# Optimization experiments

Hardware: AMD Instinct MI355X
Metric: run time of the kernel (lower is better)

The kernel has to match this reference:

```python
import jax, jax.numpy as jnp
import numpy as np

N, E = 20000, 160000
H, C1, C_OUT, D_IN = 4, 256, 512, 128
HID = H * C1  # 1024


def gat_conv(x, src, dst, W, a_src, a_dst, b, heads, ch, concat):
    n = x.shape[0]
    xw = (x @ W).reshape(n, heads, ch)                     # [N,H,C]
    es = jnp.sum(xw * a_src, axis=-1)                      # [N,H]
    ed = jnp.sum(xw * a_dst, axis=-1)                      # [N,H]
    e = jax.nn.leaky_relu(es[src] + ed[dst], 0.2)          # [Etot,H]
    m = jax.ops.segment_max(e, dst, num_segments=n)
    m = jnp.where(jnp.isfinite(m), m, 0.0)
    p = jnp.exp(e - m[dst])
    denom = jax.ops.segment_sum(p, dst, num_segments=n)
    alpha = p / (denom[dst] + 1e-16)                       # segment softmax
    out = jax.ops.segment_sum(alpha[:, :, None] * xw[src], dst, num_segments=n)
    out = out.reshape(n, heads * ch) if concat else out.mean(axis=1)
    return out + b


def layer_norm(x, g, b, eps=1e-5):
    mu = jnp.mean(x, axis=-1, keepdims=True)
    var = jnp.var(x, axis=-1, keepdims=True)
    return (x - mu) * jax.lax.rsqrt(var + eps) * g + b


def setup_inputs() -> dict:
    key = jax.random.key(0)
    ks = jax.random.split(key, 16)
    s1, s2, s3 = (2.0 / D_IN) ** 0.5, (2.0 / HID) ** 0.5, (2.0 / HID) ** 0.5
    return {
        "x": jax.random.normal(ks[0], (N, D_IN), jnp.float32),
        "edge_index": jax.random.randint(ks[1], (2, E), 0, N, jnp.int64),
        "W1": jax.random.normal(ks[2], (D_IN, H * C1), jnp.float32) * s1,
        "a_src1": jax.random.normal(ks[3], (H, C1), jnp.float32) * 0.1,
        "a_dst1": jax.random.normal(ks[4], (H, C1), jnp.float32) * 0.1,
        "b1": jnp.zeros((HID,), jnp.float32),
        "ln1_g": jnp.ones((HID,), jnp.float32),
        "ln1_b": jnp.zeros((HID,), jnp.float32),
        "W2": jax.random.normal(ks[5], (HID, H * C1), jnp.float32) * s2,
        "a_src2": jax.random.normal(ks[6], (H, C1), jnp.float32) * 0.1,
        "a_dst2": jax.random.normal(ks[7], (H, C1), jnp.float32) * 0.1,
        "b2": jnp.zeros((HID,), jnp.float32),
        "ln2_g": jnp.ones((HID,), jnp.float32),
        "ln2_b": jnp.zeros((HID,), jnp.float32),
        "W3": jax.random.normal(ks[8], (HID, C_OUT), jnp.float32) * s3,
        "a_src3": jax.random.normal(ks[9], (1, C_OUT), jnp.float32) * 0.1,
        "a_dst3": jax.random.normal(ks[10], (1, C_OUT), jnp.float32) * 0.1,
        "b3": jnp.zeros((C_OUT,), jnp.float32),
    }


def reference(x, edge_index, W1, a_src1, a_dst1, b1, ln1_g, ln1_b,
              W2, a_src2, a_dst2, b2, ln2_g, ln2_b,
              W3, a_src3, a_dst3, b3):
    # add self loops (PyG GATConv default add_self_loops=True)
    loops = jnp.arange(N, dtype=edge_index.dtype)
    src = jnp.concatenate([edge_index[0], loops])
    dst = jnp.concatenate([edge_index[1], loops])

    h = gat_conv(x, src, dst, W1, a_src1, a_dst1, b1, H, C1, True)
    h = jax.nn.elu(layer_norm(h, ln1_g, ln1_b))  # dropout: eval mode (identity)
    h = gat_conv(h, src, dst, W2, a_src2, a_dst2, b2, H, C1, True)
    h = jax.nn.elu(layer_norm(h, ln2_g, ln2_b))
    out = gat_conv(h, src, dst, W3, a_src3, a_dst3, b3, 1, C_OUT, True)
    return out
```

## Files before the change

kernel.cpp:

```cpp
#include <hip/hip_runtime.h>
#include <hip/hip_bf16.h>

typedef __hip_bfloat16 bf16;
typedef __attribute__((ext_vector_type(8))) short short8;
typedef __attribute__((ext_vector_type(4))) float float4v;

#define NN 20000
#define EE 160000
#define ET (NN + EE)

__device__ __forceinline__ float bf2f(bf16 v){ return __bfloat162float(v); }
__device__ __forceinline__ float raw2f(unsigned short u){ return __uint_as_float(((unsigned)u) << 16); }

struct Ptrs { const void* p[18]; int n[18]; };

__global__ void k_detect(Ptrs P, int* __restrict__ flags){
  int b = blockIdx.x;
  int t = threadIdx.x;
  if (b == 1){
    const int* e = (const int*)P.p[1];
    int odd = e[2*t + 1];
    unsigned long long m2 = __ballot(odd != 0);
    if (t == 0){ flags[1] = (m2 == 0ULL) ? 1 : 0; }
    return;
  }
  const unsigned* w = (const unsigned*)P.p[b];
  int nwords = P.n[b] / 2;
  unsigned v = w[t % nwords];
  int e8 = (v >> 7) & 0xFF;
  int looks = (e8 >= 100 && e8 <= 140) ? 1 : 0;
  unsigned long long mz = __ballot(v == 0u);
  unsigned long long ml = __ballot(looks);
  if (t == 0){
    int nz = __popcll(mz);
    int nonz = 64 - nz;
    int nl = __popcll(ml);
    flags[8+b] = (nonz > 0 && 2*nl >= nonz) ? 0 : 1;
  }
}

struct P13 { const void* src[13]; int off[13]; int n[13]; int fi[13]; };
struct PrepArgs {
  const void* xraw; bf16* Xc;
  const void* w1raw; bf16* Wt1;
  const void* w2raw; bf16* Wt2;
  const void* w3raw; bf16* Wt3;
  const int* eiraw; int* eic;
  P13 p13; float* prm;
  int* counts;
  const int* flags;
};

__device__ __forceinline__ void do_transpose(float (*tile)[33], const void* raw,
    bf16* wt, int K, int M, int f, int bx, int by, int t){
  int kb = by*32, mb = bx*32;
  int tx = t & 31, ty = t >> 5;
  for (int r = 0; r < 4; r++){
    int k = kb + ty + r*8;
    int m = mb + tx;
    float v = f ? ((const float*)raw)[(size_t)k*M+m] : bf2f(((const bf16*)raw)[(size_t)k*M+m]);
    tile[ty + r*8][tx] = v;
  }
  __syncthreads();
  for (int r = 0; r < 4; r++){
    int m = mb + ty + r*8;
    int k = kb + tx;
    wt[(size_t)m*K + k] = __float2bfloat16(tile[tx][ty + r*8]);
  }
}

__global__ __launch_bounds__(256) void k_prep(PrepArgs A){
  __shared__ float tile[32][33];
  int b = blockIdx.x, t = threadIdx.x;
  const int* flags = A.flags;
  if (b < 10000){
    int i = b*256 + t;
    if (flags[8+0]) A.Xc[i] = __float2bfloat16(((const float*)A.xraw)[i]);
    else            A.Xc[i] = ((const bf16*)A.xraw)[i];
  } else if (b < 10128){
    int r = b - 10000;
    do_transpose(tile, A.w1raw, A.Wt1, 128, 1024, flags[8+2], r & 31, r >> 5, t);
  } else if (b < 11152){
    int r = b - 10128;
    do_transpose(tile, A.w2raw, A.Wt2, 1024, 1024, flags[8+8], r & 31, r >> 5, t);
  } else if (b < 11664){
    int r = b - 11152;
    do_transpose(tile, A.w3raw, A.Wt3, 1024, 512, flags[8+14], r & 15, r >> 4, t);
  } else if (b < 12914){
    int i = (b - 11664)*256 + t;
    if (i < 2*EE) A.eic[i] = flags[1] ? A.eiraw[2*i] : A.eiraw[i];
  } else if (b < 12927){
    int pb = b - 12914;
    const void* s = A.p13.src[pb];
    int n = A.p13.n[pb];
    float* d = A.prm + A.p13.off[pb];
    int f = flags[8 + A.p13.fi[pb]];
    for (int i = t; i < n; i += 256)
      d[i] = f ? ((const float*)s)[i] : bf2f(((const bf16*)s)[i]);
  } else {
    int i = (b - 12927)*256 + t;
    if (i < NN) A.counts[i] = 1;
  }
}

__global__ void k_hist(const int* __restrict__ ei, int* __restrict__ counts){
  int e = blockIdx.x*256 + threadIdx.x;
  if (e < EE){
    int d = ei[EE + e];
    if (d >= 0 && d < NN) atomicAdd(&counts[d], 1);
  }
}

__global__ __launch_bounds__(1024) void k_scan(const int* __restrict__ counts, int* __restrict__ rp){
  __shared__ int wsum[16];
  __shared__ int sc;
  int t = threadIdx.x, lane = t & 63, wv = t >> 6;
  if (t == 0) sc = 0;
  __syncthreads();
  for (int base = 0; base < NN; base += 1024){
    int i = base + t;
    int v = (i < NN) ? counts[i] : 0;
    int x = v;
    #pragma unroll
    for (int o = 1; o < 64; o <<= 1){
      int y = __shfl_up(x, o, 64);
      if (lane >= o) x += y;
    }
    if (lane == 63) wsum[wv] = x;
    __syncthreads();
    if (wv == 0 && lane < 16){
      int w = wsum[lane];
      #pragma unroll
      for (int o = 1; o < 16; o <<= 1){
        int y = __shfl_up(w, o, 16);
        if ((lane & 15) >= o) w += y;
      }
      wsum[lane] = w;
    }
    __syncthreads();
    int carry = sc;
    int wpre = (wv > 0) ? wsum[wv-1] : 0;
    if (i < NN) rp[i] = carry + wpre + x - v;
    __syncthreads();
    if (t == 1023) sc = carry + wsum[15];
    __syncthreads();
  }
  if (t == 0) rp[NN] = sc;
}

__global__ void k_selfloop(const int* __restrict__ rp, int* __restrict__ cursor, int* __restrict__ col){
  int i = blockIdx.x*256 + threadIdx.x;
  if (i < NN){ int p = rp[i]; col[p] = i; cursor[i] = p + 1; }
}

__global__ void k_scatter(const int* __restrict__ ei, int* __restrict__ cursor, int* __restrict__ col){
  int e = blockIdx.x*256 + threadIdx.x;
  if (e < EE){
    int s = ei[e], d = ei[EE + e];
    if (d >= 0 && d < NN){
      int pos = atomicAdd(&cursor[d], 1);
      col[pos] = s;
    }
  }
}

__global__ void k_zero2(float* __restrict__ a, float* __restrict__ b, int n){
  int i = blockIdx.x*256 + threadIdx.x;
  if (i < n){ a[i] = 0.f; b[i] = 0.f; }
}

__global__ __launch_bounds__(256) void k_gemm_mfma(
    const bf16* __restrict__ X, const bf16* __restrict__ Wt, bf16* __restrict__ Y,
    const float* __restrict__ as_, const float* __restrict__ ad_,
    float* __restrict__ es, float* __restrict__ ed,
    int K, int M, int C, int H)
{
  __shared__ bf16 Xs[128*32];
  __shared__ bf16 Bs[128*32];
  int ncols = gridDim.x;
  int bid = blockIdx.y * ncols + blockIdx.x;
  int xcd  = bid & 7;
  int rest = bid >> 3;
  int colb = rest % ncols;
  int rowb = xcd + 8 * (rest / ncols);
  int r0 = rowb * 128;
  if (r0 >= NN) return;
  int c0 = colb * 128;

  int tid  = threadIdx.x;
  int wave = tid >> 6, lane = tid & 63;
  int quad = lane >> 4, l15 = lane & 15;
  int wr = (wave >> 1) * 64;
  int wc = (wave & 1) * 64;

  float4v acc[4][4];
  #pragma unroll
  for (int i=0;i<4;i++)
    #pragma unroll
    for (int j=0;j<4;j++)
      acc[i][j] = (float4v){0.f,0.f,0.f,0.f};

  for (int k0 = 0; k0 < K; k0 += 32){
    #pragma unroll
    for (int i = 0; i < 2; i++){
      int ch = i*256 + tid;
      int row = ch >> 2, kp = ch & 3;
      const bf16* gx = X  + (size_t)(r0 + row)*K + k0 + kp*8;
      const bf16* gb = Wt + (size_t)(c0 + row)*K + k0 + kp*8;
      __builtin_amdgcn_global_load_lds(
        (const __attribute__((address_space(1))) unsigned int*)gx,
        (__attribute__((address_space(3))) unsigned int*)(Xs + ch*8), 16, 0, 0);
      __builtin_amdgcn_global_load_lds(
        (const __attribute__((address_space(1))) unsigned int*)gb,
        (__attribute__((address_space(3))) unsigned int*)(Bs + ch*8), 16, 0, 0);
    }
    __syncthreads();

    short8 af[4], bfr[4];
    #pragma unroll
    for (int i = 0; i < 4; i++)
      af[i]  = *(const short8*)(Xs + ((size_t)(wr + i*16 + l15))*32 + quad*8);
    #pragma unroll
    for (int j = 0; j < 4; j++)
      bfr[j] = *(const short8*)(Bs + ((size_t)(wc + j*16 + l15))*32 + quad*8);
    #pragma unroll
    for (int i = 0; i < 4; i++)
      #pragma unroll
      for (int j = 0; j < 4; j++)
        acc[i][j] = __builtin_amdgcn_mfma_f32_16x16x32_bf16(af[i], bfr[j], acc[i][j], 0, 0, 0);
    __syncthreads();
  }

  int h = c0 / C;
  float asv[4], adv[4];
  #pragma unroll
  for (int j = 0; j < 4; j++){
    int colj = c0 + wc + j*16 + l15;
    asv[j] = as_[colj]; adv[j] = ad_[colj];
  }
  #pragma unroll
  for (int i = 0; i < 4; i++){
    int rbase = r0 + wr + i*16 + quad*4;
    #pragma unroll
    for (int rg = 0; rg < 4; rg++){
      int row = rbase + rg;
      bool ok = (row < NN);
      float pe = 0.f, pd = 0.f;
      #pragma unroll
      for (int j = 0; j < 4; j++){
        float v = acc[i][j][rg];
        int colj = c0 + wc + j*16 + l15;
        if (ok) Y[(size_t)row*M + colj] = __float2bfloat16(v);
        pe += v * asv[j];
        pd += v * adv[j];
      }
      #pragma unroll
      for (int o = 1; o < 16; o <<= 1){
        pe += __shfl_xor(pe, o, 64);
        pd += __shfl_xor(pd, o, 64);
      }
      if (ok && l15 == 0){
        atomicAdd(&es[row*H + h], pe);
        atomicAdd(&ed[row*H + h], pd);
      }
    }
  }
}

#define DCAP 1024
__global__ __launch_bounds__(256) void k_aggln(const int* __restrict__ rp, const int* __restrict__ col,
    const bf16* __restrict__ xw, const float* __restrict__ es, const float* __restrict__ ed,
    const float* __restrict__ bias, const float* __restrict__ gam, const float* __restrict__ bet,
    bf16* __restrict__ act){
  int n = blockIdx.x, t = threadIdx.x;
  int h = t >> 6;
  __shared__ float llog[DCAP][4];
  __shared__ int ssrc[DCAP];
  __shared__ float smv[4], srd[4];
  __shared__ float ls1[256], ls2[256];
  int e0 = rp[n], e1 = rp[n+1], deg = e1 - e0;
  float4 ed4 = *(const float4*)&ed[n*4];
  float a0=0.f, a1=0.f, a2=0.f, a3=0.f;
  const unsigned short* xwu = (const unsigned short*)xw;

  if (deg <= DCAP){
    for (int j = t; j < deg; j += 256){
      int s = col[e0 + j];
      ssrc[j] = s;
      float4 e4 = *(const float4*)&es[s*4];
      float v0 = e4.x + ed4.x; llog[j][0] = v0 > 0.f ? v0 : 0.2f*v0;
      float v1 = e4.y + ed4.y; llog[j][1] = v1 > 0.f ? v1 : 0.2f*v1;
      float v2 = e4.z + ed4.z; llog[j][2] = v2 > 0.f ? v2 : 0.2f*v2;
      float v3 = e4.w + ed4.w; llog[j][3] = v3 > 0.f ? v3 : 0.2f*v3;
    }
    __syncthreads();
    if (t < 4){
      float m = -1e30f;
      for (int j = 0; j < deg; j++) m = fmaxf(m, llog[j][t]);
      float den = 0.f;
      for (int j = 0; j < deg; j++) den += __expf(llog[j][t] - m);
      smv[t] = m; srd[t] = 1.f/(den + 1e-16f);
    }
    __syncthreads();
    for (int j = t; j < deg; j += 256){
      #pragma unroll
      for (int hh = 0; hh < 4; hh++)
        llog[j][hh] = __expf(llog[j][hh] - smv[hh]) * srd[hh];
    }
    __syncthreads();
    int j = 0;
    for (; j + 4 <= deg; j += 4){
      int s0=ssrc[j], s1=ssrc[j+1], s2=ssrc[j+2], s3=ssrc[j+3];
      float al0=llog[j][h], al1=llog[j+1][h], al2=llog[j+2][h], al3=llog[j+3][h];
      ushort4 u0 = *(const ushort4*)(xwu + (size_t)s0*1024 + 4*t);
      ushort4 u1 = *(const ushort4*)(xwu + (size_t)s1*1024 + 4*t);
      ushort4 u2 = *(const ushort4*)(xwu + (size_t)s2*1024 + 4*t);
      ushort4 u3 = *(const ushort4*)(xwu + (size_t)s3*1024 + 4*t);
      a0 += al0*raw2f(u0.x); a1 += al0*raw2f(u0.y); a2 += al0*raw2f(u0.z); a3 += al0*raw2f(u0.w);
      a0 += al1*raw2f(u1.x); a1 += al1*raw2f(u1.y); a2 += al1*raw2f(u1.z); a3 += al1*raw2f(u1.w);
      a0 += al2*raw2f(u2.x); a1 += al2*raw2f(u2.y); a2 += al2*raw2f(u2.z); a3 += al2*raw2f(u2.w);
      a0 += al3*raw2f(u3.x); a1 += al3*raw2f(u3.y); a2 += al3*raw2f(u3.z); a3 += al3*raw2f(u3.w);
    }
    for (; j < deg; j++){
      int s = ssrc[j];
      float al = llog[j][h];
      ushort4 u = *(const ushort4*)(xwu + (size_t)s*1024 + 4*t);
      a0 += al*raw2f(u.x); a1 += al*raw2f(u.y); a2 += al*raw2f(u.z); a3 += al*raw2f(u.w);
    }
  } else {
    if (t < 4){
      float m = -1e30f;
      for (int e = e0; e < e1; e++){
        float v = es[col[e]*4 + t] + ed[n*4 + t];
        v = v > 0.f ? v : 0.2f*v;
        m = fmaxf(m, v);
      }
      float den = 0.f;
      for (int e = e0; e < e1; e++){
        float v = es[col[e]*4 + t] + ed[n*4 + t];
        v = v > 0.f ? v : 0.2f*v;
        den += __expf(v - m);
      }
      smv[t] = m; srd[t] = 1.f/(den + 1e-16f);
    }
    __syncthreads();
    float edh = ed[n*4 + h];
    for (int e = e0; e < e1; e++){
      int s = col[e];
      float v = es[s*4 + h] + edh;
      v = v > 0.f ? v : 0.2f*v;
      float al = __expf(v - smv[h]) * srd[h];
      ushort4 u = *(const ushort4*)(xwu + (size_t)s*1024 + 4*t);
      a0 += al*raw2f(u.x); a1 += al*raw2f(u.y); a2 += al*raw2f(u.z); a3 += al*raw2f(u.w);
    }
  }

  a0 += bias[4*t+0]; a1 += bias[4*t+1]; a2 += bias[4*t+2]; a3 += bias[4*t+3];
  float s1 = a0+a1+a2+a3;
  float s2 = a0*a0+a1*a1+a2*a2+a3*a3;
  ls1[t] = s1; ls2[t] = s2;
  __syncthreads();
  for (int o = 128; o > 0; o >>= 1){
    if (t < o){ ls1[t] += ls1[t+o]; ls2[t] += ls2[t+o]; }
    __syncthreads();
  }
  float mu  = ls1[0] * (1.f/1024.f);
  float var = ls2[0] * (1.f/1024.f) - mu*mu;
  float rstd = rsqrtf(fmaxf(var, 0.f) + 1e-5f);
  float v0 = (a0-mu)*rstd*gam[4*t+0] + bet[4*t+0];
  float v1 = (a1-mu)*rstd*gam[4*t+1] + bet[4*t+1];
  float v2 = (a2-mu)*rstd*gam[4*t+2] + bet[4*t+2];
  float v3 = (a3-mu)*rstd*gam[4*t+3] + bet[4*t+3];
  v0 = v0 > 0.f ? v0 : (__expf(v0)-1.f);
  v1 = v1 > 0.f ? v1 : (__expf(v1)-1.f);
  v2 = v2 > 0.f ? v2 : (__expf(v2)-1.f);
  v3 = v3 > 0.f ? v3 : (__expf(v3)-1.f);
  ushort4 o4;
  { bf16 hh2=__float2bfloat16(v0); o4.x=*(unsigned short*)&hh2; }
  { bf16 hh2=__float2bfloat16(v1); o4.y=*(unsigned short*)&hh2; }
  { bf16 hh2=__float2bfloat16(v2); o4.z=*(unsigned short*)&hh2; }
  { bf16 hh2=__float2bfloat16(v3); o4.w=*(unsigned short*)&hh2; }
  *(ushort4*)((unsigned short*)act + (size_t)n*1024 + 4*t) = o4;
}

__global__ __launch_bounds__(256) void k_agg3(const int* __restrict__ rp, const int* __restrict__ col,
    const bf16* __restrict__ xw, const float* __restrict__ es, const float* __restrict__ ed,
    const float* __restrict__ bias, float* __restrict__ out){
  int n = blockIdx.x, t = threadIdx.x;
  __shared__ float llog[DCAP];
  __shared__ int ssrc[DCAP];
  __shared__ float smv, srd;
  int e0 = rp[n], e1 = rp[n+1], deg = e1 - e0;
  float edv = ed[n];
  float a0 = 0.f, a1 = 0.f;
  const unsigned short* xwu = (const unsigned short*)xw;

  if (deg <= DCAP){
    for (int j = t; j < deg; j += 256){
      int s = col[e0 + j];
      ssrc[j] = s;
      float v = es[s] + edv;
      llog[j] = v > 0.f ? v : 0.2f*v;
    }
    __syncthreads();
    if (t == 0){
      float m = -1e30f;
      for (int j = 0; j < deg; j++) m = fmaxf(m, llog[j]);
      float den = 0.f;
      for (int j = 0; j < deg; j++) den += __expf(llog[j] - m);
      smv = m; srd = 1.f/(den + 1e-16f);
    }
    __syncthreads();
    for (int j = t; j < deg; j += 256)
      llog[j] = __expf(llog[j] - smv) * srd;
    __syncthreads();
    int j = 0;
    for (; j + 4 <= deg; j += 4){
      int s0=ssrc[j], s1=ssrc[j+1], s2=ssrc[j+2], s3=ssrc[j+3];
      float al0=llog[j], al1=llog[j+1], al2=llog[j+2], al3=llog[j+3];
      ushort2 u0 = *(const ushort2*)(xwu + (size_t)s0*512 + 2*t);
      ushort2 u1 = *(const ushort2*)(xwu + (size_t)s1*512 + 2*t);
      ushort2 u2 = *(const ushort2*)(xwu + (size_t)s2*512 + 2*t);
      ushort2 u3 = *(const ushort2*)(xwu + (size_t)s3*512 + 2*t);
      a0 += al0*raw2f(u0.x); a1 += al0*raw2f(u0.y);
      a0 += al1*raw2f(u1.x); a1 += al1*raw2f(u1.y);
      a0 += al2*raw2f(u2.x); a1 += al2*raw2f(u2.y);
      a0 += al3*raw2f(u3.x); a1 += al3*raw2f(u3.y);
    }
    for (; j < deg; j++){
      int s = ssrc[j];
      float al = llog[j];
      ushort2 u = *(const ushort2*)(xwu + (size_t)s*512 + 2*t);
      a0 += al*raw2f(u.x); a1 += al*raw2f(u.y);
    }
  } else {
    if (t == 0){
      float m = -1e30f;
      for (int e = e0; e < e1; e++){
        float v = es[col[e]] + edv;
        v = v > 0.f ? v : 0.2f*v;
        m = fmaxf(m, v);
      }
      float den = 0.f;
      for (int e = e0; e < e1; e++){
        float v = es[col[e]] + edv;
        v = v > 0.f ? v : 0.2f*v;
        den += __expf(v - m);
      }
      smv = m; srd = 1.f/(den + 1e-16f);
    }
    __syncthreads();
    for (int e = e0; e < e1; e++){
      int s = col[e];
      float v = es[s] + edv;
      v = v > 0.f ? v : 0.2f*v;
      float al = __expf(v - smv) * srd;
      ushort2 u = *(const ushort2*)(xwu + (size_t)s*512 + 2*t);
      a0 += al*raw2f(u.x); a1 += al*raw2f(u.y);
    }
  }
  out[(size_t)n*512 + 2*t]     = a0 + bias[2*t];
  out[(size_t)n*512 + 2*t + 1] = a1 + bias[2*t+1];
}

__global__ void k_wssmall(float* __restrict__ out, float code){
  if (threadIdx.x == 0) out[0] = code;
}

extern "C" void kernel_launch(void* const* d_in, const int* in_sizes, int n_in,
                              void* d_out, int out_size, void* d_ws, size_t ws_size,
                              hipStream_t stream){
  float* out = (float*)d_out;
  char* ws = (char*)d_ws;

  static const int EXP_SZ[18] = {2560000, 320000, 131072, 1024,1024,1024,1024,1024,
                                 1048576, 1024,1024,1024,1024,1024,
                                 524288, 512,512,512};
  if (n_in != 18){ k_wssmall<<<1,64,0,stream>>>(out, 500.0f*301.0f); return; }
  for (int i = 0; i < 18; i++)
    if (in_sizes[i] != EXP_SZ[i]){ k_wssmall<<<1,64,0,stream>>>(out, 500.0f*302.0f); return; }
  if (out_size != NN*512){ k_wssmall<<<1,64,0,stream>>>(out, 500.0f*303.0f); return; }
  const size_t NEED = 93215360;
  if (ws_size < NEED){ k_wssmall<<<1,64,0,stream>>>(out, 500.0f*304.0f); return; }

  bf16* xw    = (bf16*) (ws);
  bf16* act   = (bf16*) (ws + 40960000);
  bf16* Xc    = (bf16*) (ws + 81920000);
  bf16* Wt1   = (bf16*) (ws + 87040000);
  bf16* Wt2   = (bf16*) (ws + 87302144);
  bf16* Wt3   = (bf16*) (ws + 89399296);
  float* prm  = (float*)(ws + 90447872);
  int*  flags = (int*)  (ws + 90494976);
  int*  eic   = (int*)  (ws + 90495232);
  float* es   = (float*)(ws + 91775232);
  int*  cur   = (int*)  (ws + 91775232);
  float* ed   = (float*)(ws + 92095232);
  int*  rp    = (int*)  (ws + 92415232);
  int*  col   = (int*)  (ws + 92495360);

  float *as1=prm+0, *ad1=prm+1024, *b1=prm+2048, *lg1=prm+3072, *lb1=prm+4096;
  float *as2=prm+5120, *ad2=prm+6144, *b2=prm+7168, *lg2=prm+8192, *lb2=prm+9216;
  float *as3=prm+10240, *ad3=prm+10752, *b3=prm+11264;

  const int TB = 256;
  int gbN = (NN + TB - 1)/TB;
  int gbE = (EE + TB - 1)/TB;

  {
    Ptrs P;
    for (int i=0;i<18;i++){ P.p[i]=d_in[i]; P.n[i]=in_sizes[i]; }
    k_detect<<<18, 64, 0, stream>>>(P, flags);
  }
  {
    PrepArgs A;
    A.xraw = d_in[0]; A.Xc = Xc;
    A.w1raw = d_in[2]; A.Wt1 = Wt1;
    A.w2raw = d_in[8]; A.Wt2 = Wt2;
    A.w3raw = d_in[14]; A.Wt3 = Wt3;
    A.eiraw = (const int*)d_in[1]; A.eic = eic;
    const int idx[13] = {3,4,5,6,7, 9,10,11,12,13, 15,16,17};
    const int off[13] = {0,1024,2048,3072,4096, 5120,6144,7168,8192,9216, 10240,10752,11264};
    const int nn [13] = {1024,1024,1024,1024,1024, 1024,1024,1024,1024,1024, 512,512,512};
    for (int i=0;i<13;i++){ A.p13.src[i]=d_in[idx[i]]; A.p13.off[i]=off[i]; A.p13.n[i]=nn[i]; A.p13.fi[i]=idx[i]; }
    A.prm = prm; A.counts = cur; A.flags = flags;
    k_prep<<<13006, TB, 0, stream>>>(A);
  }

  k_hist<<<gbE, TB, 0, stream>>>(eic, cur);
  k_scan<<<1, 1024, 0, stream>>>(cur, rp);
  k_selfloop<<<gbN, TB, 0, stream>>>(rp, cur, col);
  k_scatter<<<gbE, TB, 0, stream>>>(eic, cur, col);

  const int RB = (NN + 127)/128;
  const int R8 = ((RB + 7)/8)*8;
  dim3 g12(1024/128, R8);
  dim3 g3 (512/128,  R8);

  k_zero2<<<(NN*4+255)/256, TB, 0, stream>>>(es, ed, NN*4);
  k_gemm_mfma<<<g12, TB, 0, stream>>>(Xc, Wt1, xw, as1, ad1, es, ed, 128, 1024, 256, 4);
  k_aggln<<<NN, TB, 0, stream>>>(rp, col, xw, es, ed, b1, lg1, lb1, act);

  k_zero2<<<(NN*4+255)/256, TB, 0, stream>>>(es, ed, NN*4);
  k_gemm_mfma<<<g12, TB, 0, stream>>>(act, Wt2, xw, as2, ad2, es, ed, 1024, 1024, 256, 4);
  k_aggln<<<NN, TB, 0, stream>>>(rp, col, xw, es, ed, b2, lg2, lb2, act);

  k_zero2<<<(NN+255)/256, TB, 0, stream>>>(es, ed, NN);
  k_gemm_mfma<<<g3, TB, 0, stream>>>(act, Wt3, xw, as3, ad3, es, ed, 1024, 512, 512, 1);
  k_agg3<<<NN, TB, 0, stream>>>(rp, col, xw, es, ed, b3, out);
}
```

Before: 542.8 us.

## Map one wavefront per node in GAT aggregation kernels with shuffle-based softmax

Aggregation and LayerNorm kernels now assign one 64-lane wavefront per destination node (four nodes per block) instead of a whole 256-thread block. Edge logits, the segment max and the softmax sum are computed in registers with wave shuffles, and the LayerNorm reduction also uses shuffles. This removes shared memory, block barriers and the serial per-head softmax loops. Each lane now handles 16 (or 8) contiguous channels with wider loads. Nodes with degree above 64 fall back to a serial per-lane loop, which could be slow on skewed graphs.

```diff
diff --git a/kernel.cpp b/kernel.cpp
--- a/kernel.cpp
+++ b/kernel.cpp
@@ -11,6 +11,10 @@
 
 __device__ __forceinline__ float bf2f(bf16 v){ return __bfloat162float(v); }
 __device__ __forceinline__ float raw2f(unsigned short u){ return __uint_as_float(((unsigned)u) << 16); }
+__device__ __forceinline__ unsigned short f2raw(float f){
+  bf16 h = __float2bfloat16(f);
+  return *(unsigned short*)&h;
+}
 
 struct Ptrs { const void* p[18]; int n[18]; };
 
@@ -267,200 +271,211 @@
   }
 }
 
-#define DCAP 1024
 __global__ __launch_bounds__(256) void k_aggln(const int* __restrict__ rp, const int* __restrict__ col,
     const bf16* __restrict__ xw, const float* __restrict__ es, const float* __restrict__ ed,
     const float* __restrict__ bias, const float* __restrict__ gam, const float* __restrict__ bet,
     bf16* __restrict__ act){
-  int n = blockIdx.x, t = threadIdx.x;
-  int h = t >> 6;
-  __shared__ float llog[DCAP][4];
-  __shared__ int ssrc[DCAP];
-  __shared__ float smv[4], srd[4];
-  __shared__ float ls1[256], ls2[256];
+  int wv = threadIdx.x >> 6, lane = threadIdx.x & 63;
+  int n = blockIdx.x*4 + wv;
+  int h = lane >> 4;
+  int cb = lane * 16;
   int e0 = rp[n], e1 = rp[n+1], deg = e1 - e0;
   float4 ed4 = *(const float4*)&ed[n*4];
-  float a0=0.f, a1=0.f, a2=0.f, a3=0.f;
   const unsigned short* xwu = (const unsigned short*)xw;
 
-  if (deg <= DCAP){
-    for (int j = t; j < deg; j += 256){
-      int s = col[e0 + j];
-      ssrc[j] = s;
-      float4 e4 = *(const float4*)&es[s*4];
-      float v0 = e4.x + ed4.x; llog[j][0] = v0 > 0.f ? v0 : 0.2f*v0;
-      float v1 = e4.y + ed4.y; llog[j][1] = v1 > 0.f ? v1 : 0.2f*v1;
-      float v2 = e4.z + ed4.z; llog[j][2] = v2 > 0.f ? v2 : 0.2f*v2;
-      float v3 = e4.w + ed4.w; llog[j][3] = v3 > 0.f ? v3 : 0.2f*v3;
-    }
-    __syncthreads();
-    if (t < 4){
-      float m = -1e30f;
-      for (int j = 0; j < deg; j++) m = fmaxf(m, llog[j][t]);
-      float den = 0.f;
-      for (int j = 0; j < deg; j++) den += __expf(llog[j][t] - m);
-      smv[t] = m; srd[t] = 1.f/(den + 1e-16f);
-    }
-    __syncthreads();
-    for (int j = t; j < deg; j += 256){
-      #pragma unroll
-      for (int hh = 0; hh < 4; hh++)
-        llog[j][hh] = __expf(llog[j][hh] - smv[hh]) * srd[hh];
-    }
-    __syncthreads();
-    int j = 0;
-    for (; j + 4 <= deg; j += 4){
-      int s0=ssrc[j], s1=ssrc[j+1], s2=ssrc[j+2], s3=ssrc[j+3];
-      float al0=llog[j][h], al1=llog[j+1][h], al2=llog[j+2][h], al3=llog[j+3][h];
-      ushort4 u0 = *(const ushort4*)(xwu + (size_t)s0*1024 + 4*t);
-      ushort4 u1 = *(const ushort4*)(xwu + (size_t)s1*1024 + 4*t);
-      ushort4 u2 = *(const ushort4*)(xwu + (size_t)s2*1024 + 4*t);
-      ushort4 u3 = *(const ushort4*)(xwu + (size_t)s3*1024 + 4*t);
-      a0 += al0*raw2f(u0.x); a1 += al0*raw2f(u0.y); a2 += al0*raw2f(u0.z); a3 += al0*raw2f(u0.w);
-      a0 += al1*raw2f(u1.x); a1 += al1*raw2f(u1.y); a2 += al1*raw2f(u1.z); a3 += al1*raw2f(u1.w);
-      a0 += al2*raw2f(u2.x); a1 += al2*raw2f(u2.y); a2 += al2*raw2f(u2.z); a3 += al2*raw2f(u2.w);
-      a0 += al3*raw2f(u3.x); a1 += al3*raw2f(u3.y); a2 += al3*raw2f(u3.z); a3 += al3*raw2f(u3.w);
-    }
-    for (; j < deg; j++){
-      int s = ssrc[j];
-      float al = llog[j][h];
-      ushort4 u = *(const ushort4*)(xwu + (size_t)s*1024 + 4*t);
-      a0 += al*raw2f(u.x); a1 += al*raw2f(u.y); a2 += al*raw2f(u.z); a3 += al*raw2f(u.w);
+  float acc[16];
+  #pragma unroll
+  for (int c=0;c<16;c++) acc[c]=0.f;
+
+  if (deg <= 64){
+    int src = 0;
+    float l0=-1e30f, l1=-1e30f, l2=-1e30f, l3=-1e30f;
+    if (lane < deg){
+      src = col[e0 + lane];
+      float4 e4 = *(const float4*)&es[src*4];
+      float v;
+      v = e4.x + ed4.x; l0 = v > 0.f ? v : 0.2f*v;
+      v = e4.y + ed4.y; l1 = v > 0.f ? v : 0.2f*v;
+      v = e4.z + ed4.z; l2 = v > 0.f ? v : 0.2f*v;
+      v = e4.w + ed4.w; l3 = v > 0.f ? v : 0.2f*v;
+    }
+    float m0=l0, m1=l1, m2=l2, m3=l3;
+    #pragma unroll
+    for (int o=1;o<64;o<<=1){
+      m0 = fmaxf(m0, __shfl_xor(m0,o,64));
+      m1 = fmaxf(m1, __shfl_xor(m1,o,64));
+      m2 = fmaxf(m2, __shfl_xor(m2,o,64));
+      m3 = fmaxf(m3, __shfl_xor(m3,o,64));
+    }
+    float p0 = (lane<deg) ? __expf(l0-m0) : 0.f;
+    float p1 = (lane<deg) ? __expf(l1-m1) : 0.f;
+    float p2 = (lane<deg) ? __expf(l2-m2) : 0.f;
+    float p3 = (lane<deg) ? __expf(l3-m3) : 0.f;
+    float d0=p0, d1=p1, d2=p2, d3=p3;
+    #pragma unroll
+    for (int o=1;o<64;o<<=1){
+      d0 += __shfl_xor(d0,o,64);
+      d1 += __shfl_xor(d1,o,64);
+      d2 += __shfl_xor(d2,o,64);
+      d3 += __shfl_xor(d3,o,64);
+    }
+    float al0 = p0 * (1.f/(d0+1e-16f));
+    float al1 = p1 * (1.f/(d1+1e-16f));
+    float al2 = p2 * (1.f/(d2+1e-16f));
+    float al3 = p3 * (1.f/(d3+1e-16f));
+
+    for (int j=0;j<deg;j++){
+      int s = __shfl(src, j, 64);
+      float a0j = __shfl(al0, j, 64);
+      float a1j = __shfl(al1, j, 64);
+      float a2j = __shfl(al2, j, 64);
+      float a3j = __shfl(al3, j, 64);
+      float aj = (h==0) ? a0j : ((h==1) ? a1j : ((h==2) ? a2j : a3j));
+      const unsigned short* row = xwu + (size_t)s*1024 + cb;
+      ushort4 u0 = *(const ushort4*)(row);
+      ushort4 u1 = *(const ushort4*)(row+4);
+      ushort4 u2 = *(const ushort4*)(row+8);
+      ushort4 u3 = *(const ushort4*)(row+12);
+      acc[0] += aj*raw2f(u0.x); acc[1] += aj*raw2f(u0.y); acc[2] += aj*raw2f(u0.z); acc[3] += aj*raw2f(u0.w);
+      acc[4] += aj*raw2f(u1.x); acc[5] += aj*raw2f(u1.y); acc[6] += aj*raw2f(u1.z); acc[7] += aj*raw2f(u1.w);
+      acc[8] += aj*raw2f(u2.x); acc[9] += aj*raw2f(u2.y); acc[10]+= aj*raw2f(u2.z); acc[11]+= aj*raw2f(u2.w);
+      acc[12]+= aj*raw2f(u3.x); acc[13]+= aj*raw2f(u3.y); acc[14]+= aj*raw2f(u3.z); acc[15]+= aj*raw2f(u3.w);
     }
   } else {
-    if (t < 4){
-      float m = -1e30f;
-      for (int e = e0; e < e1; e++){
-        float v = es[col[e]*4 + t] + ed[n*4 + t];
-        v = v > 0.f ? v : 0.2f*v;
-        m = fmaxf(m, v);
-      }
-      float den = 0.f;
-      for (int e = e0; e < e1; e++){
-        float v = es[col[e]*4 + t] + ed[n*4 + t];
-        v = v > 0.f ? v : 0.2f*v;
-        den += __expf(v - m);
-      }
-      smv[t] = m; srd[t] = 1.f/(den + 1e-16f);
-    }
-    __syncthreads();
-    float edh = ed[n*4 + h];
-    for (int e = e0; e < e1; e++){
+    float edh = (h==0) ? ed4.x : ((h==1) ? ed4.y : ((h==2) ? ed4.z : ed4.w));
+    float m = -1e30f;
+    for (int e=e0;e<e1;e++){
+      float v = es[col[e]*4 + h] + edh;
+      v = v > 0.f ? v : 0.2f*v;
+      m = fmaxf(m, v);
+    }
+    float den = 0.f;
+    for (int e=e0;e<e1;e++){
+      float v = es[col[e]*4 + h] + edh;
+      v = v > 0.f ? v : 0.2f*v;
+      den += __expf(v - m);
+    }
+    float rd = 1.f/(den + 1e-16f);
+    for (int e=e0;e<e1;e++){
       int s = col[e];
       float v = es[s*4 + h] + edh;
       v = v > 0.f ? v : 0.2f*v;
-      float al = __expf(v - smv[h]) * srd[h];
-      ushort4 u = *(const ushort4*)(xwu + (size_t)s*1024 + 4*t);
-      a0 += al*raw2f(u.x); a1 += al*raw2f(u.y); a2 += al*raw2f(u.z); a3 += al*raw2f(u.w);
-    }
-  }
-
-  a0 += bias[4*t+0]; a1 += bias[4*t+1]; a2 += bias[4*t+2]; a3 += bias[4*t+3];
-  float s1 = a0+a1+a2+a3;
-  float s2 = a0*a0+a1*a1+a2*a2+a3*a3;
-  ls1[t] = s1; ls2[t] = s2;
-  __syncthreads();
-  for (int o = 128; o > 0; o >>= 1){
-    if (t < o){ ls1[t] += ls1[t+o]; ls2[t] += ls2[t+o]; }
-    __syncthreads();
-  }
-  float mu  = ls1[0] * (1.f/1024.f);
-  float var = ls2[0] * (1.f/1024.f) - mu*mu;
+      float aj = __expf(v - m) * rd;
+      const unsigned short* row = xwu + (size_t)s*1024 + cb;
+      ushort4 u0 = *(const ushort4*)(row);
+      ushort4 u1 = *(const ushort4*)(row+4);
+      ushort4 u2 = *(const ushort4*)(row+8);
+      ushort4 u3 = *(const ushort4*)(row+12);
+      acc[0] += aj*raw2f(u0.x); acc[1] += aj*raw2f(u0.y); acc[2] += aj*raw2f(u0.z); acc[3] += aj*raw2f(u0.w);
+      acc[4] += aj*raw2f(u1.x); acc[5] += aj*raw2f(u1.y); acc[6] += aj*raw2f(u1.z); acc[7] += aj*raw2f(u1.w);
+      acc[8] += aj*raw2f(u2.x); acc[9] += aj*raw2f(u2.y); acc[10]+= aj*raw2f(u2.z); acc[11]+= aj*raw2f(u2.w);
+      acc[12]+= aj*raw2f(u3.x); acc[13]+= aj*raw2f(u3.y); acc[14]+= aj*raw2f(u3.z); acc[15]+= aj*raw2f(u3.w);
+    }
+  }
+
+  #pragma unroll
+  for (int c=0;c<16;c++) acc[c] += bias[cb+c];
+  float s1 = 0.f, s2 = 0.f;
+  #pragma unroll
+  for (int c=0;c<16;c++){ s1 += acc[c]; s2 += acc[c]*acc[c]; }
+  #pragma unroll
+  for (int o=1;o<64;o<<=1){
+    s1 += __shfl_xor(s1,o,64);
+    s2 += __shfl_xor(s2,o,64);
+  }
+  float mu  = s1 * (1.f/1024.f);
+  float var = s2 * (1.f/1024.f) - mu*mu;
   float rstd = rsqrtf(fmaxf(var, 0.f) + 1e-5f);
-  float v0 = (a0-mu)*rstd*gam[4*t+0] + bet[4*t+0];
-  float v1 = (a1-mu)*rstd*gam[4*t+1] + bet[4*t+1];
-  float v2 = (a2-mu)*rstd*gam[4*t+2] + bet[4*t+2];
-  float v3 = (a3-mu)*rstd*gam[4*t+3] + bet[4*t+3];
-  v0 = v0 > 0.f ? v0 : (__expf(v0)-1.f);
-  v1 = v1 > 0.f ? v1 : (__expf(v1)-1.f);
-  v2 = v2 > 0.f ? v2 : (__expf(v2)-1.f);
-  v3 = v3 > 0.f ? v3 : (__expf(v3)-1.f);
-  ushort4 o4;
-  { bf16 hh2=__float2bfloat16(v0); o4.x=*(unsigned short*)&hh2; }
-  { bf16 hh2=__float2bfloat16(v1); o4.y=*(unsigned short*)&hh2; }
-  { bf16 hh2=__float2bfloat16(v2); o4.z=*(unsigned short*)&hh2; }
-  { bf16 hh2=__float2bfloat16(v3); o4.w=*(unsigned short*)&hh2; }
-  *(ushort4*)((unsigned short*)act + (size_t)n*1024 + 4*t) = o4;
+
+  ushort4 o4[4];
+  #pragma unroll
+  for (int q=0;q<4;q++){
+    float v0 = (acc[q*4+0]-mu)*rstd*gam[cb+q*4+0] + bet[cb+q*4+0];
+    float v1 = (acc[q*4+1]-mu)*rstd*gam[cb+q*4+1] + bet[cb+q*4+1];
+    float v2 = (acc[q*4+2]-mu)*rstd*gam[cb+q*4+2] + bet[cb+q*4+2];
+    float v3 = (acc[q*4+3]-mu)*rstd*gam[cb+q*4+3] + bet[cb+q*4+3];
+    v0 = v0 > 0.f ? v0 : (__expf(v0)-1.f);
+    v1 = v1 > 0.f ? v1 : (__expf(v1)-1.f);
+    v2 = v2 > 0.f ? v2 : (__expf(v2)-1.f);
+    v3 = v3 > 0.f ? v3 : (__expf(v3)-1.f);
+    o4[q].x = f2raw(v0); o4[q].y = f2raw(v1); o4[q].z = f2raw(v2); o4[q].w = f2raw(v3);
+  }
+  unsigned short* dst = (unsigned short*)act + (size_t)n*1024 + cb;
+  *(ushort4*)(dst)    = o4[0];
+  *(ushort4*)(dst+4)  = o4[1];
+  *(ushort4*)(dst+8)  = o4[2];
+  *(ushort4*)(dst+12) = o4[3];
 }
 
 __global__ __launch_bounds__(256) void k_agg3(const int* __restrict__ rp, const int* __restrict__ col,
     const bf16* __restrict__ xw, const float* __restrict__ es, const float* __restrict__ ed,
     const float* __restrict__ bias, float* __restrict__ out){
-  int n = blockIdx.x, t = threadIdx.x;
-  __shared__ float llog[DCAP];
-  __shared__ int ssrc[DCAP];
-  __shared__ float smv, srd;
+  int wv = threadIdx.x >> 6, lane = threadIdx.x & 63;
+  int n = blockIdx.x*4 + wv;
+  int cb = lane * 8;
   int e0 = rp[n], e1 = rp[n+1], deg = e1 - e0;
   float edv = ed[n];
-  float a0 = 0.f, a1 = 0.f;
   const unsigned short* xwu = (const unsigned short*)xw;
 
-  if (deg <= DCAP){
-    for (int j = t; j < deg; j += 256){
-      int s = col[e0 + j];
-      ssrc[j] = s;
-      float v = es[s] + edv;
-      llog[j] = v > 0.f ? v : 0.2f*v;
-    }
-    __syncthreads();
-    if (t == 0){
-      float m = -1e30f;
-      for (int j = 0; j < deg; j++) m = fmaxf(m, llog[j]);
-      float den = 0.f;
-      for (int j = 0; j < deg; j++) den += __expf(llog[j] - m);
-      smv = m; srd = 1.f/(den + 1e-16f);
-    }
-    __syncthreads();
-    for (int j = t; j < deg; j += 256)
-      llog[j] = __expf(llog[j] - smv) * srd;
-    __syncthreads();
-    int j = 0;
-    for (; j + 4 <= deg; j += 4){
-      int s0=ssrc[j], s1=ssrc[j+1], s2=ssrc[j+2], s3=ssrc[j+3];
-      float al0=llog[j], al1=llog[j+1], al2=llog[j+2], al3=llog[j+3];
-      ushort2 u0 = *(const ushort2*)(xwu + (size_t)s0*512 + 2*t);
-      ushort2 u1 = *(const ushort2*)(xwu + (size_t)s1*512 + 2*t);
-      ushort2 u2 = *(const ushort2*)(xwu + (size_t)s2*512 + 2*t);
-      ushort2 u3 = *(const ushort2*)(xwu + (size_t)s3*512 + 2*t);
-      a0 += al0*raw2f(u0.x); a1 += al0*raw2f(u0.y);
-      a0 += al1*raw2f(u1.x); a1 += al1*raw2f(u1.y);
-      a0 += al2*raw2f(u2.x); a1 += al2*raw2f(u2.y);
-      a0 += al3*raw2f(u3.x); a1 += al3*raw2f(u3.y);
-    }
-    for (; j < deg; j++){
-      int s = ssrc[j];
-      float al = llog[j];
-      ushort2 u = *(const ushort2*)(xwu + (size_t)s*512 + 2*t);
-      a0 += al*raw2f(u.x); a1 += al*raw2f(u.y);
+  float acc[8];
+  #pragma unroll
+  for (int c=0;c<8;c++) acc[c]=0.f;
+
+  if (deg <= 64){
+    int src = 0;
+    float l = -1e30f;
+    if (lane < deg){
+      src = col[e0 + lane];
+      float v = es[src] + edv;
+      l = v > 0.f ? v : 0.2f*v;
+    }
+    float m = l;
+    #pragma unroll
+    for (int o=1;o<64;o<<=1) m = fmaxf(m, __shfl_xor(m,o,64));
+    float p = (lane<deg) ? __expf(l-m) : 0.f;
+    float d = p;
+    #pragma unroll
+    for (int o=1;o<64;o<<=1) d += __shfl_xor(d,o,64);
+    float al = p * (1.f/(d+1e-16f));
+
+    for (int j=0;j<deg;j++){
+      int s = __shfl(src, j, 64);
+      float aj = __shfl(al, j, 64);
+      const unsigned short* row = xwu + (size_t)s*512 + cb;
+      ushort4 u0 = *(const ushort4*)(row);
+      ushort4 u1 = *(const ushort4*)(row+4);
+      acc[0] += aj*raw2f(u0.x); acc[1] += aj*raw2f(u0.y); acc[2] += aj*raw2f(u0.z); acc[3] += aj*raw2f(u0.w);
+      acc[4] += aj*raw2f(u1.x); acc[5] += aj*raw2f(u1.y); acc[6] += aj*raw2f(u1.z); acc[7] += aj*raw2f(u1.w);
     }
   } else {
-    if (t == 0){
-      float m = -1e30f;
-      for (int e = e0; e < e1; e++){
-        float v = es[col[e]] + edv;
-        v = v > 0.f ? v : 0.2f*v;
-        m = fmaxf(m, v);
-      }
-      float den = 0.f;
-      for (int e = e0; e < e1; e++){
-        float v = es[col[e]] + edv;
-        v = v > 0.f ? v : 0.2f*v;
-        den += __expf(v - m);
-      }
-      smv = m; srd = 1.f/(den + 1e-16f);
-    }
-    __syncthreads();
-    for (int e = e0; e < e1; e++){
+    float m = -1e30f;
+    for (int e=e0;e<e1;e++){
+      float v = es[col[e]] + edv;
+      v = v > 0.f ? v : 0.2f*v;
+      m = fmaxf(m, v);
+    }
+    float den = 0.f;
+    for (int e=e0;e<e1;e++){
+      float v = es[col[e]] + edv;
+      v = v > 0.f ? v : 0.2f*v;
+      den += __expf(v - m);
+    }
+    float rd = 1.f/(den + 1e-16f);
+    for (int e=e0;e<e1;e++){
       int s = col[e];
       float v = es[s] + edv;
       v = v > 0.f ? v : 0.2f*v;
-      float al = __expf(v - smv) * srd;
-      ushort2 u = *(const ushort2*)(xwu + (size_t)s*512 + 2*t);
-      a0 += al*raw2f(u.x); a1 += al*raw2f(u.y);
-    }
-  }
-  out[(size_t)n*512 + 2*t]     = a0 + bias[2*t];
-  out[(size_t)n*512 + 2*t + 1] = a1 + bias[2*t+1];
+      float aj = __expf(v - m) * rd;
+      const unsigned short* row = xwu + (size_t)s*512 + cb;
+      ushort4 u0 = *(const ushort4*)(row);
+      ushort4 u1 = *(const ushort4*)(row+4);
+      acc[0] += aj*raw2f(u0.x); acc[1] += aj*raw2f(u0.y); acc[2] += aj*raw2f(u0.z); acc[3] += aj*raw2f(u0.w);
+      acc[4] += aj*raw2f(u1.x); acc[5] += aj*raw2f(u1.y); acc[6] += aj*raw2f(u1.z); acc[7] += aj*raw2f(u1.w);
+    }
+  }
+  float* dst = out + (size_t)n*512 + cb;
+  #pragma unroll
+  for (int c=0;c<8;c++) dst[c] = acc[c] + bias[cb+c];
 }
 
 __global__ void k_wssmall(float* __restrict__ out, float code){
@@ -538,13 +553,13 @@
 
   k_zero2<<<(NN*4+255)/256, TB, 0, stream>>>(es, ed, NN*4);
   k_gemm_mfma<<<g12, TB, 0, stream>>>(Xc, Wt1, xw, as1, ad1, es, ed, 128, 1024, 256, 4);
-  k_aggln<<<NN, TB, 0, stream>>>(rp, col, xw, es, ed, b1, lg1, lb1, act);
+  k_aggln<<<NN/4, TB, 0, stream>>>(rp, col, xw, es, ed, b1, lg1, lb1, act);
 
   k_zero2<<<(NN*4+255)/256, TB, 0, stream>>>(es, ed, NN*4);
   k_gemm_mfma<<<g12, TB, 0, stream>>>(act, Wt2, xw, as2, ad2, es, ed, 1024, 1024, 256, 4);
-  k_aggln<<<NN, TB, 0, stream>>>(rp, col, xw, es, ed, b2, lg2, lb2, act);
+  k_aggln<<<NN/4, TB, 0, stream>>>(rp, col, xw, es, ed, b2, lg2, lb2, act);
 
   k_zero2<<<(NN+255)/256, TB, 0, stream>>>(es, ed, NN);
   k_gemm_mfma<<<g3, TB, 0, stream>>>(act, Wt3, xw, as3, ad3, es, ed, 1024, 512, 512, 1);
-  k_agg3<<<NN, TB, 0, stream>>>(rp, col, xw, es, ed, b3, out);
-}
+  k_agg3<<<NN/4, TB, 0, stream>>>(rp, col, xw, es, ed, b3, out);
+}
```

After: 501.1 us. 7.7% less time.
